# Kernel optimization log

Hardware: AMD Instinct MI355X
Metric: run time of the kernel (lower is better)

The kernel has to match this reference:

```python
import jax, jax.numpy as jnp
import numpy as np

N_NODES = 100000
N_EDGES = 600000
IN_DIM, HID_DIM, OUT_DIM = 128, 128, 128
NEG_SLOPE = 0.2  # PyG GATConv default


def _glorot(key, shape):
    fan = sum(shape)
    lim = jnp.sqrt(6.0 / fan)
    return jax.random.uniform(key, shape, jnp.float32, -lim, lim)


def setup_inputs() -> dict:
    key = jax.random.key(0)
    ks = jax.random.split(key, 10)
    x = jax.random.normal(ks[0], (N_NODES, IN_DIM), jnp.float32)
    edge_index = jax.random.randint(ks[1], (2, N_EDGES), 0, N_NODES, jnp.int64)
    return {
        "x": x,
        "edge_index": edge_index,
        "W1": _glorot(ks[2], (IN_DIM, HID_DIM)),
        "a_src1": _glorot(ks[3], (HID_DIM,)),
        "a_dst1": _glorot(ks[4], (HID_DIM,)),
        "b1": jnp.zeros((HID_DIM,), jnp.float32),
        "W2": _glorot(ks[5], (HID_DIM, OUT_DIM)),
        "a_src2": _glorot(ks[6], (OUT_DIM,)),
        "a_dst2": _glorot(ks[7], (OUT_DIM,)),
        "b2": jnp.zeros((OUT_DIM,), jnp.float32),
    }


def _gat_conv(x, src, dst, W, a_src, a_dst, b, n_nodes):
    """Single-head PyG-style GATConv (concat=True, heads=1, with self-loops already in src/dst)."""
    h = x @ W                                   # [N, F]
    alpha_s = h @ a_src                         # [N]
    alpha_d = h @ a_dst                         # [N]
    e = jax.nn.leaky_relu(alpha_s[src] + alpha_d[dst], NEG_SLOPE)  # [E]
    # segment softmax over incoming edges of each dst node
    m = jax.lax.stop_gradient(jax.ops.segment_max(e, dst, num_segments=n_nodes))
    w = jnp.exp(e - m[dst])                     # [E]
    denom = jax.ops.segment_sum(w, dst, num_segments=n_nodes)  # [N]
    alpha = w / denom[dst]                      # [E]
    out = jax.ops.segment_sum(h[src] * alpha[:, None], dst, num_segments=n_nodes)
    return out + b


def reference(x, edge_index, W1, a_src1, a_dst1, b1, W2, a_src2, a_dst2, b2):
    n = x.shape[0]
    loop = jnp.arange(n, dtype=edge_index.dtype)
    src = jnp.concatenate([edge_index[0], loop])  # add self-loops (PyG default)
    dst = jnp.concatenate([edge_index[1], loop])
    h = jax.nn.relu(_gat_conv(x, src, dst, W1, a_src1, a_dst1, b1, n))
    out = _gat_conv(h, src, dst, W2, a_src2, a_dst2, b2, n)
    return out.mean(axis=0)  # [out_dim]
```

## Files before the change

### kernel.cpp

```cpp
#include <hip/hip_runtime.h>


#define NEG_SLOPE 0.2f

typedef __attribute__((ext_vector_type(8))) short bf16x8;
typedef __attribute__((ext_vector_type(4))) float f32x4;

__device__ __forceinline__ float leaky(float x) { return x > 0.0f ? x : NEG_SLOPE * x; }

__device__ __forceinline__ unsigned int bf16rne(float f) {
  unsigned int u = __float_as_uint(f);
  return (u + 0x7fffu + ((u >> 16) & 1u)) >> 16;
}
__device__ __forceinline__ unsigned int packbf(float a, float b) {
  return bf16rne(a) | (bf16rne(b) << 16);
}
__device__ __forceinline__ float bf_lo(unsigned int u) { return __uint_as_float(u << 16); }
__device__ __forceinline__ float bf_hi(unsigned int u) { return __uint_as_float(u & 0xffff0000u); }

__device__ __forceinline__ void accum8(float* a, float w, uint4 h) {
  a[0] += w * bf_lo(h.x); a[1] += w * bf_hi(h.x);
  a[2] += w * bf_lo(h.y); a[3] += w * bf_hi(h.y);
  a[4] += w * bf_lo(h.z); a[5] += w * bf_hi(h.z);
  a[6] += w * bf_lo(h.w); a[7] += w * bf_hi(h.w);
}

__device__ __forceinline__ float2 gat_node2(
    const uint4* __restrict__ H4, const float* __restrict__ vas,
    const float* __restrict__ vad, const int* __restrict__ fill,
    const int* __restrict__ esrcp, const int2* __restrict__ ovf,
    const int* __restrict__ ovfn, int node0, int node1, int nclamp,
    int lane, int l, float* acc0, float* acc1) {
  int t0 = esrcp[(size_t)node0 * 16 + l];
  int t1 = esrcp[(size_t)node1 * 16 + l];
  int dg0 = fill[node0];
  int dg1 = fill[node1];
  float ad0 = vad[node0], ad1 = vad[node1];
  float as0 = vas[node0], as1 = vas[node1];
  uint4 hs0 = H4[(size_t)node0 * 16 + l];
  uint4 hs1 = H4[(size_t)node1 * 16 + l];
  int u0 = min(max(t0, 0), nclamp);
  int u1 = min(max(t1, 0), nclamp);
  float vs0 = vas[u0];
  float vs1 = vas[u1];
  uint4 hb0[8], hb1[8];
#pragma unroll
  for (int i = 0; i < 8; i++) {
    int ut = __shfl(u0, (lane & 48) + i, 64);
    hb0[i] = H4[(size_t)ut * 16 + l];
  }
#pragma unroll
  for (int i = 0; i < 8; i++) {
    int ut = __shfl(u1, (lane & 48) + i, 64);
    hb1[i] = H4[(size_t)ut * 16 + l];
  }
  const bool big0 = dg0 > 8, big1 = dg1 > 8;
  uint4 hc0[8];
  if (big0) {
#pragma unroll
    for (int i = 0; i < 8; i++) {
      int ut = __shfl(u0, (lane & 48) + 8 + i, 64);
      hc0[i] = H4[(size_t)ut * 16 + l];
    }
  }
  float es0 = leaky(as0 + ad0), es1 = leaky(as1 + ad1);
  float wj0 = (l < dg0) ? __expf(leaky(vs0 + ad0) - es0) : 0.f;
  float wj1 = (l < dg1) ? __expf(leaky(vs1 + ad1) - es1) : 0.f;
  float ds0 = wj0, ds1 = wj1;
#pragma unroll
  for (int o = 8; o; o >>= 1) ds0 += __shfl_xor(ds0, o, 16);
#pragma unroll
  for (int o = 8; o; o >>= 1) ds1 += __shfl_xor(ds1, o, 16);
#pragma unroll
  for (int i = 0; i < 8; i++) {
    float w = __shfl(wj0, (lane & 48) + i, 64);
    accum8(acc0, w, hb0[i]);
  }
  if (big0) {
#pragma unroll
    for (int i = 0; i < 8; i++) {
      float w = __shfl(wj0, (lane & 48) + 8 + i, 64);
      accum8(acc0, w, hc0[i]);
    }
  }
  uint4 hc1[8];
  if (big1) {
#pragma unroll
    for (int i = 0; i < 8; i++) {
      int ut = __shfl(u1, (lane & 48) + 8 + i, 64);
      hc1[i] = H4[(size_t)ut * 16 + l];
    }
  }
#pragma unroll
  for (int i = 0; i < 8; i++) {
    float w = __shfl(wj1, (lane & 48) + i, 64);
    accum8(acc1, w, hb1[i]);
  }
  if (big1) {
#pragma unroll
    for (int i = 0; i < 8; i++) {
      float w = __shfl(wj1, (lane & 48) + 8 + i, 64);
      accum8(acc1, w, hc1[i]);
    }
  }
  if (dg0 > 16 || dg1 > 16) {
    int ovn = *ovfn;
    for (int k = 0; k < ovn; k++) {
      int2 ent = ovf[k];
      if (ent.x == node0) {
        float w = __expf(leaky(vas[ent.y] + ad0) - es0);
        ds0 += w;
        accum8(acc0, w, H4[(size_t)ent.y * 16 + l]);
      }
      if (ent.x == node1) {
        float w = __expf(leaky(vas[ent.y] + ad1) - es1);
        ds1 += w;
        accum8(acc1, w, H4[(size_t)ent.y * 16 + l]);
      }
    }
  }
  accum8(acc0, 1.0f, hs0);
  accum8(acc1, 1.0f, hs1);
  return make_float2(1.0f / (ds0 + 1.0f), 1.0f / (ds1 + 1.0f));
}

__global__ __launch_bounds__(256) void setup_k(const float* __restrict__ W1,
                                               const float* __restrict__ W2,
                                               unsigned short* __restrict__ Wf1,
                                               unsigned short* __restrict__ Wf2,
                                               int* __restrict__ fill,
                                               float* __restrict__ c,
                                               int* __restrict__ esrcp,
                                               int* __restrict__ ovfn,
                                               float* __restrict__ partial,
                                               int n, int nfb) {
  const int b = blockIdx.x;
  if (b < 2) {
    const float* W = b ? W2 : W1;
    unsigned short* Wf = b ? Wf2 : Wf1;
    for (int idx = threadIdx.x; idx < 16384; idx += 256) {
      int j = idx & 7;
      int lane = (idx >> 3) & 63;
      int fid = idx >> 9;
      int ct = fid >> 2, ks = fid & 3;
      int q = lane >> 4, l15 = lane & 15;
      Wf[idx] = (unsigned short)bf16rne(W[(ks * 32 + q * 8 + j) * 128 + ct * 16 + l15]);
    }
    return;
  }
  if (b == 2) {
    for (int i = threadIdx.x; i < 64 * 128; i += 256) partial[i] = 0.f;
    if (threadIdx.x == 0) *ovfn = 0;
    return;
  }
  if (b < 3 + nfb) {
    int base = (b - 3) * 1024 + threadIdx.x * 4;
#pragma unroll
    for (int i = 0; i < 4; i++)
      if (base + i < n) {
        fill[base + i] = 0;
        c[base + i] = 0.f;
      }
    return;
  }
  size_t base = (size_t)(b - 3 - nfb) * 1024 + threadIdx.x * 4;
  size_t tot = (size_t)n * 16;
  if (base + 4 <= tot) {
    *(int4*)&esrcp[base] = make_int4(0, 0, 0, 0);
  } else {
    for (size_t i = base; i < tot; i++) esrcp[i] = 0;
  }
}

__global__ void scatter_kernel(const int* __restrict__ src, const int* __restrict__ dst,
                               int* __restrict__ fill, int* __restrict__ esrcp,
                               int2* __restrict__ ovf, int* __restrict__ ovfn, int E) {
  int e = blockIdx.x * 256 + threadIdx.x;
  if (e < E) {
    int v = dst[e];
    int sv = src[e];
    int p = atomicAdd(&fill[v], 1);
    if (p < 16) {
      esrcp[(size_t)v * 16 + p] = sv;
    } else {
      int k = atomicAdd(ovfn, 1);
      ovf[k] = make_int2(v, sv);
    }
  }
}

__device__ __forceinline__ void cvt_f32(const float4* raw, bf16x8* xf) {
#pragma unroll
  for (int ks = 0; ks < 4; ks++) {
    union { bf16x8 v; unsigned int u[4]; } cv;
    cv.u[0] = packbf(raw[2 * ks].x, raw[2 * ks].y);
    cv.u[1] = packbf(raw[2 * ks].z, raw[2 * ks].w);
    cv.u[2] = packbf(raw[2 * ks + 1].x, raw[2 * ks + 1].y);
    cv.u[3] = packbf(raw[2 * ks + 1].z, raw[2 * ks + 1].w);
    xf[ks] = cv.v;
  }
}

__device__ __forceinline__ void mfma_tile(const unsigned short* WL, const bf16x8* xf,
                                          const float* __restrict__ a_s,
                                          const float* __restrict__ a_d,
                                          unsigned short* __restrict__ H,
                                          float* __restrict__ vas,
                                          float* __restrict__ vad, int myrow, bool act,
                                          int lane, int q) {
  f32x4 acc[8];
#pragma unroll
  for (int ct = 0; ct < 8; ct++) acc[ct] = (f32x4){0.f, 0.f, 0.f, 0.f};
#pragma unroll
  for (int ks = 0; ks < 4; ks++) {
    bf16x8 wf[8];
#pragma unroll
    for (int ct = 0; ct < 8; ct++)
      wf[ct] = *(const bf16x8*)&WL[(((ct << 2) + ks) << 9) + lane * 8];
#pragma unroll
    for (int ct = 0; ct < 8; ct++)
      acc[ct] = __builtin_amdgcn_mfma_f32_16x16x32_bf16(wf[ct], xf[ks], acc[ct], 0, 0, 0);
  }
  float ds = 0.f, dd = 0.f;
#pragma unroll
  for (int ct = 0; ct < 8; ct++) {
    const int c0 = ct * 16 + q * 4;
    float4 as4 = *(const float4*)&a_s[c0];
    float4 ad4 = *(const float4*)&a_d[c0];
    ds += acc[ct][0] * as4.x + acc[ct][1] * as4.y + acc[ct][2] * as4.z + acc[ct][3] * as4.w;
    dd += acc[ct][0] * ad4.x + acc[ct][1] * ad4.y + acc[ct][2] * ad4.z + acc[ct][3] * ad4.w;
    if (act) {
      uint2 o;
      o.x = packbf(acc[ct][0], acc[ct][1]);
      o.y = packbf(acc[ct][2], acc[ct][3]);
      *(uint2*)&H[(size_t)myrow * 128 + c0] = o;
    }
  }
  ds += __shfl_xor(ds, 16, 64);
  ds += __shfl_xor(ds, 32, 64);
  dd += __shfl_xor(dd, 16, 64);
  dd += __shfl_xor(dd, 32, 64);
  if (q == 0 && act) {
    vas[myrow] = ds;
    vad[myrow] = dd;
  }
}

__global__ __launch_bounds__(256) void gemm_mfma1(const float* __restrict__ Xf,
                                                  const unsigned short* __restrict__ Wf,
                                                  const float* __restrict__ a_s,
                                                  const float* __restrict__ a_d,
                                                  unsigned short* __restrict__ H,
                                                  float* __restrict__ vas,
                                                  float* __restrict__ vad, int n,
                                                  int nt16, int ngemm) {
  __shared__ unsigned short WL[32 * 512];
  const int lane = threadIdx.x & 63;
  const int wv = threadIdx.x >> 6;
  const int l15 = lane & 15;
  const int q = lane >> 4;
  const int t0 = blockIdx.x * 4 + wv;
  const int t1 = t0 + ngemm * 4;
  const int r0 = t0 * 16 + l15;
  const int r1 = t1 * 16 + l15;
  const bool wact0 = t0 < nt16;
  const bool wact1 = t1 < nt16;
  const bool act0 = wact0 && (r0 < n);
  const bool act1 = wact1 && (r1 < n);

  float4 raw0[8];
  if (wact0) {
#pragma unroll
    for (int ks = 0; ks < 4; ks++) {
      float4 z = {0.f, 0.f, 0.f, 0.f};
      raw0[2 * ks] = z;
      raw0[2 * ks + 1] = z;
      if (act0) {
        raw0[2 * ks] = *(const float4*)&Xf[(size_t)r0 * 128 + ks * 32 + q * 8];
        raw0[2 * ks + 1] = *(const float4*)&Xf[(size_t)r0 * 128 + ks * 32 + q * 8 + 4];
      }
    }
  }
  {
    const uint4* __restrict__ Wg4 = (const uint4*)Wf;
    uint4* WL4 = (uint4*)WL;
#pragma unroll
    for (int j = 0; j < 8; j++) WL4[threadIdx.x + 256 * j] = Wg4[threadIdx.x + 256 * j];
  }
  __syncthreads();
  if (!wact0) return;

  float4 raw1[8];
  if (wact1) {
#pragma unroll
    for (int ks = 0; ks < 4; ks++) {
      float4 z = {0.f, 0.f, 0.f, 0.f};
      raw1[2 * ks] = z;
      raw1[2 * ks + 1] = z;
      if (act1) {
        raw1[2 * ks] = *(const float4*)&Xf[(size_t)r1 * 128 + ks * 32 + q * 8];
        raw1[2 * ks + 1] = *(const float4*)&Xf[(size_t)r1 * 128 + ks * 32 + q * 8 + 4];
      }
    }
  }

  bf16x8 xf[4];
  cvt_f32(raw0, xf);
  mfma_tile(WL, xf, a_s, a_d, H, vas, vad, r0, act0, lane, q);
  if (wact1) {
    cvt_f32(raw1, xf);
    mfma_tile(WL, xf, a_s, a_d, H, vas, vad, r1, act1, lane, q);
  }
}

__global__ __launch_bounds__(256, 3) void agg1_gemm2(
    const unsigned short* __restrict__ HA, const float* __restrict__ vas1,
    const float* __restrict__ vad1, const int* __restrict__ fill,
    const int* __restrict__ esrcp, const int2* __restrict__ ovf,
    const int* __restrict__ ovfn, const float* __restrict__ b1,
    const unsigned short* __restrict__ Wf2, const float* __restrict__ a_s2,
    const float* __restrict__ a_d2, unsigned short* __restrict__ HB,
    float* __restrict__ vas2, float* __restrict__ vad2, int n) {
  __shared__ unsigned short Atile[32 * 128];
  __shared__ float sdot[2][2][4][16];
  const int tid = threadIdx.x;
  const int lane = tid & 63;
  const int wv = tid >> 6;
  const int q = lane >> 4;
  const int l = lane & 15;
  const int row = wv * 4 + q;
  const int base = blockIdx.x * 32;
  const int node0 = base + row;
  const int node1 = base + row + 16;
  const bool valid0 = node0 < n, valid1 = node1 < n;
  const int n0s = valid0 ? node0 : n - 1;
  const int n1s = valid1 ? node1 : n - 1;
  const uint4* __restrict__ H4 = (const uint4*)HA;

  float acc0[8], acc1[8];
#pragma unroll
  for (int k = 0; k < 8; k++) { acc0[k] = 0.f; acc1[k] = 0.f; }
  float2 inv = gat_node2(H4, vas1, vad1, fill, esrcp, ovf, ovfn, n0s, n1s, n - 1,
                         lane, l, acc0, acc1);

  float4 b0 = *(const float4*)&b1[8 * l];
  float4 b1v = *(const float4*)&b1[8 * l + 4];
  uint4 o0 = {0u, 0u, 0u, 0u}, o1 = {0u, 0u, 0u, 0u};
  if (valid0) {
    float r0_ = fmaxf(acc0[0] * inv.x + b0.x, 0.f), r1_ = fmaxf(acc0[1] * inv.x + b0.y, 0.f);
    float r2_ = fmaxf(acc0[2] * inv.x + b0.z, 0.f), r3_ = fmaxf(acc0[3] * inv.x + b0.w, 0.f);
    float r4_ = fmaxf(acc0[4] * inv.x + b1v.x, 0.f), r5_ = fmaxf(acc0[5] * inv.x + b1v.y, 0.f);
    float r6_ = fmaxf(acc0[6] * inv.x + b1v.z, 0.f), r7_ = fmaxf(acc0[7] * inv.x + b1v.w, 0.f);
    o0.x = packbf(r0_, r1_); o0.y = packbf(r2_, r3_);
    o0.z = packbf(r4_, r5_); o0.w = packbf(r6_, r7_);
  }
  if (valid1) {
    float r0_ = fmaxf(acc1[0] * inv.y + b0.x, 0.f), r1_ = fmaxf(acc1[1] * inv.y + b0.y, 0.f);
    float r2_ = fmaxf(acc1[2] * inv.y + b0.z, 0.f), r3_ = fmaxf(acc1[3] * inv.y + b0.w, 0.f);
    float r4_ = fmaxf(acc1[4] * inv.y + b1v.x, 0.f), r5_ = fmaxf(acc1[5] * inv.y + b1v.y, 0.f);
    float r6_ = fmaxf(acc1[6] * inv.y + b1v.z, 0.f), r7_ = fmaxf(acc1[7] * inv.y + b1v.w, 0.f);
    o1.x = packbf(r0_, r1_); o1.y = packbf(r2_, r3_);
    o1.z = packbf(r4_, r5_); o1.w = packbf(r6_, r7_);
  }
  *(uint4*)&Atile[row * 128 + ((l ^ (row & 7)) << 3)] = o0;
  *(uint4*)&Atile[(row + 16) * 128 + ((l ^ (row & 7)) << 3)] = o1;
  __syncthreads();

  const int ct0 = 2 * wv, ct1 = 2 * wv + 1;
  f32x4 aA0 = {0.f, 0.f, 0.f, 0.f}, aB0 = aA0, aA1 = aA0, aB1 = aA0;
#pragma unroll
  for (int ks = 0; ks < 4; ks++) {
    bf16x8 w0 = *(const bf16x8*)&Wf2[(((ct0 << 2) + ks) << 9) + lane * 8];
    bf16x8 w1 = *(const bf16x8*)&Wf2[(((ct1 << 2) + ks) << 9) + lane * 8];
    bf16x8 x0 = *(const bf16x8*)&Atile[l * 128 + ((((ks << 2) + q) ^ (l & 7)) << 3)];
    bf16x8 x1 = *(const bf16x8*)&Atile[(16 + l) * 128 + ((((ks << 2) + q) ^ (l & 7)) << 3)];
    aA0 = __builtin_amdgcn_mfma_f32_16x16x32_bf16(w0, x0, aA0, 0, 0, 0);
    aB0 = __builtin_amdgcn_mfma_f32_16x16x32_bf16(w1, x0, aB0, 0, 0, 0);
    aA1 = __builtin_amdgcn_mfma_f32_16x16x32_bf16(w0, x1, aA1, 0, 0, 0);
    aB1 = __builtin_amdgcn_mfma_f32_16x16x32_bf16(w1, x1, aB1, 0, 0, 0);
  }

#pragma unroll
  for (int t = 0; t < 2; t++) {
    f32x4 aA = t ? aA1 : aA0;
    f32x4 aB = t ? aB1 : aB0;
    const int myrow = base + t * 16 + l;
    const bool ract = myrow < n;
    float ds = 0.f, dd = 0.f;
    {
      const int c0 = ct0 * 16 + q * 4;
      float4 as4 = *(const float4*)&a_s2[c0];
      float4 ad4 = *(const float4*)&a_d2[c0];
      ds += aA[0] * as4.x + aA[1] * as4.y + aA[2] * as4.z + aA[3] * as4.w;
      dd += aA[0] * ad4.x + aA[1] * ad4.y + aA[2] * ad4.z + aA[3] * ad4.w;
      if (ract) {
        uint2 ov;
        ov.x = packbf(aA[0], aA[1]);
        ov.y = packbf(aA[2], aA[3]);
        *(uint2*)&HB[(size_t)myrow * 128 + c0] = ov;
      }
    }
    {
      const int c0 = ct1 * 16 + q * 4;
      float4 as4 = *(const float4*)&a_s2[c0];
      float4 ad4 = *(const float4*)&a_d2[c0];
      ds += aB[0] * as4.x + aB[1] * as4.y + aB[2] * as4.z + aB[3] * as4.w;
      dd += aB[0] * ad4.x + aB[1] * ad4.y + aB[2] * ad4.z + aB[3] * ad4.w;
      if (ract) {
        uint2 ov;
        ov.x = packbf(aB[0], aB[1]);
        ov.y = packbf(aB[2], aB[3]);
        *(uint2*)&HB[(size_t)myrow * 128 + c0] = ov;
      }
    }
    ds += __shfl_xor(ds, 16, 64);
    ds += __shfl_xor(ds, 32, 64);
    dd += __shfl_xor(dd, 16, 64);
    dd += __shfl_xor(dd, 32, 64);
    if (q == 0) {
      sdot[t][0][wv][l] = ds;
      sdot[t][1][wv][l] = dd;
    }
  }
  __syncthreads();
  if (tid < 32) {
    int t = tid >> 4, i = tid & 15;
    int nn = base + tid;
    if (nn < n) {
      vas2[nn] = sdot[t][0][0][i] + sdot[t][0][1][i] + sdot[t][0][2][i] + sdot[t][0][3][i];
      vad2[nn] = sdot[t][1][0][i] + sdot[t][1][1][i] + sdot[t][1][2][i] + sdot[t][1][3][i];
    }
  }
}

__global__ __launch_bounds__(256) void attn2_k(const float* __restrict__ vas,
                                               const float* __restrict__ vad,
                                               const int* __restrict__ fill,
                                               const int* __restrict__ esrcp,
                                               const int2* __restrict__ ovf,
                                               const int* __restrict__ ovfn,
                                               float* __restrict__ c, int n) {
  const int tid = threadIdx.x;
  const int lane = tid & 63;
  const int l = lane & 15;
  const int node = (blockIdx.x * 256 + tid) >> 4;
  if (node >= n) return;
  int traw = esrcp[(size_t)node * 16 + l];
  int dg = fill[node];
  float adv = vad[node];
  float asv = vas[node];
  int u = min(max(traw, 0), n - 1);
  float vsr = vas[u];
  float es = leaky(asv + adv);
  const int dc = min(dg, 16);
  float w = (l < dc) ? __expf(leaky(vsr + adv) - es) : 0.f;
  float ds = w;
#pragma unroll
  for (int o = 8; o; o >>= 1) ds += __shfl_xor(ds, o, 16);
  float denom = ds + 1.0f;
  if (dg > 16) {
    int ovn = *ovfn;
    float extra = 0.f;
    for (int k = l; k < ovn; k += 16) {
      int2 ent = ovf[k];
      if (ent.x == node) extra += __expf(leaky(vas[ent.y] + adv) - es);
    }
#pragma unroll
    for (int o = 8; o; o >>= 1) extra += __shfl_xor(extra, o, 16);
    denom += extra;
  }
  const float inv = 1.0f / denom;
  if (l < dc) atomicAdd(&c[u], w * inv);
  if (l == 0) atomicAdd(&c[node], inv);
  if (dg > 16) {
    int ovn = *ovfn;
    for (int k = l; k < ovn; k += 16) {
      int2 ent = ovf[k];
      if (ent.x == node) {
        float w2 = __expf(leaky(vas[ent.y] + adv) - es);
        atomicAdd(&c[ent.y], w2 * inv);
      }
    }
  }
}

__global__ __launch_bounds__(256) void wsum_k(const unsigned short* __restrict__ HB,
                                              const float* __restrict__ c,
                                              float* __restrict__ partial, int n,
                                              int nwaves) {
  const int lane = threadIdx.x & 63;
  const int wid = blockIdx.x * 4 + (threadIdx.x >> 6);
  const unsigned int* __restrict__ H1 = (const unsigned int*)HB;
  float a0 = 0.f, a1 = 0.f;
  for (int node = wid; node < n; node += nwaves) {
    float cv = c[node];
    unsigned int h = H1[(size_t)node * 64 + lane];
    a0 += cv * bf_lo(h);
    a1 += cv * bf_hi(h);
  }
  atomicAdd(&partial[(wid & 63) * 128 + 2 * lane], a0);
  atomicAdd(&partial[(wid & 63) * 128 + 2 * lane + 1], a1);
}

__global__ void finalize_k(const float* __restrict__ partial,
                           const float* __restrict__ b2, float* __restrict__ out,
                           float invn) {
  int col = threadIdx.x;
  float s = 0.f;
#pragma unroll 8
  for (int r = 0; r < 64; r++) s += partial[r * 128 + col];
  out[col] = s * invn + b2[col];
}

extern "C" void kernel_launch(void* const* d_in, const int* in_sizes, int n_in,
                              void* d_out, int out_size, void* d_ws, size_t ws_size,
                              hipStream_t stream) {
  const float* x = (const float*)d_in[0];
  const int* ei = (const int*)d_in[1];
  const float* W1 = (const float*)d_in[2];
  const float* a_src1 = (const float*)d_in[3];
  const float* a_dst1 = (const float*)d_in[4];
  const float* b1 = (const float*)d_in[5];
  const float* W2 = (const float*)d_in[6];
  const float* a_src2 = (const float*)d_in[7];
  const float* a_dst2 = (const float*)d_in[8];
  const float* b2 = (const float*)d_in[9];
  float* out = (float*)d_out;

  const int N = in_sizes[0] / 128;
  const int E = in_sizes[1] / 2;
  const int* src = ei;
  const int* dst = ei + E;

  const size_t rowpadded = (size_t)(N + 256) * 128;

  char* p = (char*)d_ws;
  unsigned short* HA = (unsigned short*)p; p += rowpadded * 2;
  unsigned short* HB = (unsigned short*)p; p += rowpadded * 2;
  float* vas1 = (float*)p;    p += (size_t)N * 4;
  float* vad1 = (float*)p;    p += (size_t)N * 4;
  float* vas2 = (float*)p;    p += (size_t)N * 4;
  float* vad2 = (float*)p;    p += (size_t)N * 4;
  int* fill = (int*)p;        p += (size_t)N * 4;
  float* cw = (float*)p;      p += (size_t)N * 4;
  int* esrcp = (int*)p;       p += (size_t)N * 16 * 4;
  int2* ovf = (int2*)p;       p += (size_t)E * 8;
  int* ovfn = (int*)p;        p += 16;
  float* partial = (float*)p; p += 64 * 128 * 4;
  unsigned short* Wf1 = (unsigned short*)p; p += 16384 * 2;
  unsigned short* Wf2 = (unsigned short*)p; p += 16384 * 2;

  const int eblocks = (E + 255) / 256;
  const int nt16 = (N + 15) / 16;
  const int ngemm = (nt16 + 7) / 8;
  const int aggblocks = (N + 31) / 32;
  const int nfb = (N + 1023) / 1024;
  const int neb = (N * 16 + 1023) / 1024;
  const int a2blocks = (N + 15) / 16;
  const int nwaves = 2048;

  setup_k<<<3 + nfb + neb, 256, 0, stream>>>(W1, W2, Wf1, Wf2, fill, cw, esrcp, ovfn,
                                             partial, N, nfb);
  scatter_kernel<<<eblocks, 256, 0, stream>>>(src, dst, fill, esrcp, ovf, ovfn, E);
  gemm_mfma1<<<ngemm, 256, 0, stream>>>(x, Wf1, a_src1, a_dst1, HA, vas1, vad1, N, nt16, ngemm);
  agg1_gemm2<<<aggblocks, 256, 0, stream>>>(HA, vas1, vad1, fill, esrcp, ovf, ovfn, b1,
                                            Wf2, a_src2, a_dst2, HB, vas2, vad2, N);
  attn2_k<<<a2blocks, 256, 0, stream>>>(vas2, vad2, fill, esrcp, ovf, ovfn, cw, N);
  wsum_k<<<nwaves / 4, 256, 0, stream>>>(HB, cw, partial, N, nwaves);
  finalize_k<<<1, 128, 0, stream>>>(partial, b2, out, 1.0f / (float)N);
}
```

Baseline: 260.7 us.

## Cut kernel launches: memset workspace, fuse weight pack into scatter, fuse finalize

New measurement: 316.6 us. +21.5%, slower.

```diff
diff --git a/kernel.cpp b/kernel.cpp
--- a/kernel.cpp
+++ b/kernel.cpp
@@ -124,20 +124,16 @@
   return make_float2(1.0f / (ds0 + 1.0f), 1.0f / (ds1 + 1.0f));
 }
 
-__global__ __launch_bounds__(256) void setup_k(const float* __restrict__ W1,
-                                               const float* __restrict__ W2,
-                                               unsigned short* __restrict__ Wf1,
-                                               unsigned short* __restrict__ Wf2,
-                                               int* __restrict__ fill,
-                                               float* __restrict__ c,
-                                               int* __restrict__ esrcp,
-                                               int* __restrict__ ovfn,
-                                               float* __restrict__ partial,
-                                               int n, int nfb) {
+__global__ void scatter_pack(const int* __restrict__ src, const int* __restrict__ dst,
+                             int* __restrict__ fill, int* __restrict__ esrcp,
+                             int2* __restrict__ ovf, int* __restrict__ ovfn,
+                             const float* __restrict__ W1, const float* __restrict__ W2,
+                             unsigned short* __restrict__ Wf1,
+                             unsigned short* __restrict__ Wf2, int E, int eblocks) {
   const int b = blockIdx.x;
-  if (b < 2) {
-    const float* W = b ? W2 : W1;
-    unsigned short* Wf = b ? Wf2 : Wf1;
+  if (b >= eblocks) {
+    const float* W = (b == eblocks) ? W1 : W2;
+    unsigned short* Wf = (b == eblocks) ? Wf1 : Wf2;
     for (int idx = threadIdx.x; idx < 16384; idx += 256) {
       int j = idx & 7;
       int lane = (idx >> 3) & 63;
@@ -148,34 +144,7 @@
     }
     return;
   }
-  if (b == 2) {
-    for (int i = threadIdx.x; i < 64 * 128; i += 256) partial[i] = 0.f;
-    if (threadIdx.x == 0) *ovfn = 0;
-    return;
-  }
-  if (b < 3 + nfb) {
-    int base = (b - 3) * 1024 + threadIdx.x * 4;
-#pragma unroll
-    for (int i = 0; i < 4; i++)
-      if (base + i < n) {
-        fill[base + i] = 0;
-        c[base + i] = 0.f;
-      }
-    return;
-  }
-  size_t base = (size_t)(b - 3 - nfb) * 1024 + threadIdx.x * 4;
-  size_t tot = (size_t)n * 16;
-  if (base + 4 <= tot) {
-    *(int4*)&esrcp[base] = make_int4(0, 0, 0, 0);
-  } else {
-    for (size_t i = base; i < tot; i++) esrcp[i] = 0;
-  }
-}
-
-__global__ void scatter_kernel(const int* __restrict__ src, const int* __restrict__ dst,
-                               int* __restrict__ fill, int* __restrict__ esrcp,
-                               int2* __restrict__ ovf, int* __restrict__ ovfn, int E) {
-  int e = blockIdx.x * 256 + threadIdx.x;
+  int e = b * 256 + threadIdx.x;
   if (e < E) {
     int v = dst[e];
     int sv = src[e];
@@ -484,32 +453,52 @@
   }
 }
 
-__global__ __launch_bounds__(256) void wsum_k(const unsigned short* __restrict__ HB,
-                                              const float* __restrict__ c,
-                                              float* __restrict__ partial, int n,
-                                              int nwaves) {
-  const int lane = threadIdx.x & 63;
-  const int wid = blockIdx.x * 4 + (threadIdx.x >> 6);
+#define WSUM_WAVES 4096
+__global__ __launch_bounds__(256) void wsum_fin(const unsigned short* __restrict__ HB,
+                                                const float* __restrict__ c,
+                                                float* __restrict__ partial,
+                                                const float* __restrict__ b2,
+                                                float* __restrict__ out,
+                                                int* __restrict__ done, int n,
+                                                float invn) {
+  const int tid = threadIdx.x;
+  const int lane = tid & 63;
+  const int wid = blockIdx.x * 4 + (tid >> 6);
   const unsigned int* __restrict__ H1 = (const unsigned int*)HB;
   float a0 = 0.f, a1 = 0.f;
-  for (int node = wid; node < n; node += nwaves) {
-    float cv = c[node];
-    unsigned int h = H1[(size_t)node * 64 + lane];
-    a0 += cv * bf_lo(h);
-    a1 += cv * bf_hi(h);
+  for (int b = wid; b < n; b += 4 * WSUM_WAVES) {
+    const int i0 = b, i1 = b + WSUM_WAVES, i2 = b + 2 * WSUM_WAVES, i3 = b + 3 * WSUM_WAVES;
+    float c0 = c[i0];
+    float c1 = (i1 < n) ? c[i1] : 0.f;
+    float c2 = (i2 < n) ? c[i2] : 0.f;
+    float c3 = (i3 < n) ? c[i3] : 0.f;
+    unsigned int h0 = H1[(size_t)i0 * 64 + lane];
+    unsigned int h1 = (i1 < n) ? H1[(size_t)i1 * 64 + lane] : 0u;
+    unsigned int h2 = (i2 < n) ? H1[(size_t)i2 * 64 + lane] : 0u;
+    unsigned int h3 = (i3 < n) ? H1[(size_t)i3 * 64 + lane] : 0u;
+    a0 += c0 * bf_lo(h0) + c1 * bf_lo(h1) + c2 * bf_lo(h2) + c3 * bf_lo(h3);
+    a1 += c0 * bf_hi(h0) + c1 * bf_hi(h1) + c2 * bf_hi(h2) + c3 * bf_hi(h3);
   }
   atomicAdd(&partial[(wid & 63) * 128 + 2 * lane], a0);
   atomicAdd(&partial[(wid & 63) * 128 + 2 * lane + 1], a1);
-}
-
-__global__ void finalize_k(const float* __restrict__ partial,
-                           const float* __restrict__ b2, float* __restrict__ out,
-                           float invn) {
-  int col = threadIdx.x;
-  float s = 0.f;
+
+  __shared__ int islast;
+  __threadfence();
+  __syncthreads();
+  if (tid == 0) {
+    int v = atomicAdd(done, 1);
+    islast = (v == (int)gridDim.x - 1) ? 1 : 0;
+  }
+  __syncthreads();
+  if (islast) {
+    __threadfence();
+    if (tid < 128) {
+      float s = 0.f;
 #pragma unroll 8
-  for (int r = 0; r < 64; r++) s += partial[r * 128 + col];
-  out[col] = s * invn + b2[col];
+      for (int r = 0; r < 64; r++) s += partial[r * 128 + tid];
+      out[tid] = s * invn + b2[tid];
+    }
+  }
 }
 
 extern "C" void kernel_launch(void* const* d_in, const int* in_sizes, int n_in,
@@ -535,18 +524,21 @@
   const size_t rowpadded = (size_t)(N + 256) * 128;
 
   char* p = (char*)d_ws;
+  char* zstart = p;
+  int* fill = (int*)p;        p += (size_t)N * 4;
+  float* cw = (float*)p;      p += (size_t)N * 4;
+  float* partial = (float*)p; p += 64 * 128 * 4;
+  int* done = (int*)p;        p += 16;
+  int* ovfn = (int*)p;        p += 16;
+  int* esrcp = (int*)p;       p += (size_t)N * 16 * 4;
+  const size_t zsize = (size_t)(p - zstart);
   unsigned short* HA = (unsigned short*)p; p += rowpadded * 2;
   unsigned short* HB = (unsigned short*)p; p += rowpadded * 2;
   float* vas1 = (float*)p;    p += (size_t)N * 4;
   float* vad1 = (float*)p;    p += (size_t)N * 4;
   float* vas2 = (float*)p;    p += (size_t)N * 4;
   float* vad2 = (float*)p;    p += (size_t)N * 4;
-  int* fill = (int*)p;        p += (size_t)N * 4;
-  float* cw = (float*)p;      p += (size_t)N * 4;
-  int* esrcp = (int*)p;       p += (size_t)N * 16 * 4;
   int2* ovf = (int2*)p;       p += (size_t)E * 8;
-  int* ovfn = (int*)p;        p += 16;
-  float* partial = (float*)p; p += 64 * 128 * 4;
   unsigned short* Wf1 = (unsigned short*)p; p += 16384 * 2;
   unsigned short* Wf2 = (unsigned short*)p; p += 16384 * 2;
 
@@ -554,18 +546,15 @@
   const int nt16 = (N + 15) / 16;
   const int ngemm = (nt16 + 7) / 8;
   const int aggblocks = (N + 31) / 32;
-  const int nfb = (N + 1023) / 1024;
-  const int neb = (N * 16 + 1023) / 1024;
   const int a2blocks = (N + 15) / 16;
-  const int nwaves = 2048;
-
-  setup_k<<<3 + nfb + neb, 256, 0, stream>>>(W1, W2, Wf1, Wf2, fill, cw, esrcp, ovfn,
-                                             partial, N, nfb);
-  scatter_kernel<<<eblocks, 256, 0, stream>>>(src, dst, fill, esrcp, ovf, ovfn, E);
+
+  hipMemsetAsync(zstart, 0, zsize, stream);
+  scatter_pack<<<eblocks + 2, 256, 0, stream>>>(src, dst, fill, esrcp, ovf, ovfn,
+                                                W1, W2, Wf1, Wf2, E, eblocks);
   gemm_mfma1<<<ngemm, 256, 0, stream>>>(x, Wf1, a_src1, a_dst1, HA, vas1, vad1, N, nt16, ngemm);
   agg1_gemm2<<<aggblocks, 256, 0, stream>>>(HA, vas1, vad1, fill, esrcp, ovf, ovfn, b1,
                                             Wf2, a_src2, a_dst2, HB, vas2, vad2, N);
   attn2_k<<<a2blocks, 256, 0, stream>>>(vas2, vad2, fill, esrcp, ovf, ovfn, cw, N);
-  wsum_k<<<nwaves / 4, 256, 0, stream>>>(HB, cw, partial, N, nwaves);
-  finalize_k<<<1, 128, 0, stream>>>(partial, b2, out, 1.0f / (float)N);
-}
+  wsum_fin<<<WSUM_WAVES / 4, 256, 0, stream>>>(HB, cw, partial, b2, out, done, N,
+                                               1.0f / (float)N);
+}
```
